# Kernel tuning notes

Measured on AMD Instinct MI355X. Metric: run time of the kernel, lower is better.

## Reference

```python
import jax, jax.numpy as jnp
import numpy as np

B, N, L = 64, 512, 768
M, K, H = 24, 30, 1024


def setup_inputs() -> dict:
    key = jax.random.key(0)
    ks = jax.random.split(key, 7)
    sent_embedding = jax.random.normal(ks[0], (B, N, L), dtype=jnp.float32)
    entity_embedding = jax.random.normal(ks[1], (B, M, K, H), dtype=jnp.float32)
    entity_embedding_mask = jax.random.bernoulli(ks[2], 0.1, (B, M, K))
    # -1 denotes a padded (absent) alias, as handled by select_alias_word_sent
    start_span_idx = jax.random.randint(ks[3], (B, M), -1, N, dtype=jnp.int32)
    end_span_idx = jax.random.randint(ks[4], (B, M), -1, N, dtype=jnp.int32)
    W_span = jax.random.normal(ks[5], (2 * L, H), dtype=jnp.float32) * (1.0 / np.sqrt(2 * L))
    b_span = jnp.zeros((H,), dtype=jnp.float32)
    return {
        "sent_embedding": sent_embedding,
        "entity_embedding": entity_embedding,
        "entity_embedding_mask": entity_embedding_mask,
        "start_span_idx": start_span_idx,
        "end_span_idx": end_span_idx,
        "W_span": W_span,
        "b_span": b_span,
    }


def _select_alias_word_sent(idx, sent):
    # idx: (B, M) positions into sentence; -1 means padded alias -> zero vector
    pad = idx == -1                                   # (B, M)
    safe = jnp.where(pad, 0, idx)                     # (B, M)
    g = jnp.take_along_axis(sent, safe[:, :, None], axis=1)  # (B, M, L)
    return jnp.where(pad[:, :, None], 0.0, g)


def reference(sent_embedding, entity_embedding, entity_embedding_mask,
              start_span_idx, end_span_idx, W_span, b_span):
    # gather start/end word vectors of each alias span
    start_w = _select_alias_word_sent(start_span_idx, sent_embedding)  # (B, M, L)
    end_w = _select_alias_word_sent(end_span_idx, sent_embedding)      # (B, M, L)
    pair = jnp.concatenate([start_w, end_w], axis=-1)                  # (B, M, 2L)
    # span_proj: single linear layer 2L -> H
    alias_emb = pair @ W_span + b_span                                 # (B, M, H)
    # zero out masked candidates
    ent = jnp.where(entity_embedding_mask[..., None], 0.0, entity_embedding)  # (B,M,K,H)
    # per-candidate dot product (the tiny bmm in the original)
    final_scores = jnp.einsum("bmh,bmkh->bmk", alias_emb, ent)         # (B, M, K)
    return final_scores, ent
```

## Files before the change

### kernel.cpp

```cpp
#include <hip/hip_runtime.h>
#include <stdint.h>

#define B_   64
#define N_   512
#define L_   768
#define M_   24
#define K_   30
#define H_   1024
#define L2_  1536
#define BM_  (B_ * M_)
#define BMK_ (B_ * M_ * K_)

typedef __attribute__((ext_vector_type(8))) short bf16x8;
typedef __attribute__((ext_vector_type(4))) float f32x4;

__device__ __forceinline__ ushort f2bf(float f) {
    union { float f; uint32_t u; } v; v.f = f;
    uint32_t u = v.u + 0x7FFFu + ((v.u >> 16) & 1u);
    return (ushort)(u >> 16);
}

__global__ void detect_mask_kernel(const uint32_t* __restrict__ mw,
                                   int* __restrict__ flag) {
    __shared__ int f;
    if (threadIdx.x == 0) f = 0;
    __syncthreads();
    int local = 0;
    const int nw = BMK_ / 4;
    for (int i = threadIdx.x; i < nw; i += blockDim.x) {
        uint32_t v = mw[i];
        if (v != 0u && v != 1u && v != 0x3F800000u) local = 1;
    }
    if (local) f = 1;
    __syncthreads();
    if (threadIdx.x == 0) *flag = f;
}

__global__ __launch_bounds__(192) void gather_pair_bf16(
    const float* __restrict__ sent,
    const int*   __restrict__ sidx,
    const int*   __restrict__ eidx,
    ushort*      __restrict__ pairB) {

    const int bm = blockIdx.x;
    const int t  = threadIdx.x;
    const int l  = t * 8;
    const int b  = bm / M_;

    int idx, ll;
    if (l < L_) { idx = sidx[bm]; ll = l; }
    else        { idx = eidx[bm]; ll = l - L_; }

    float4 v0 = make_float4(0.f, 0.f, 0.f, 0.f), v1 = v0;
    if (idx >= 0) {
        const float* src = sent + ((size_t)(b * N_ + idx)) * L_ + ll;
        v0 = *reinterpret_cast<const float4*>(src);
        v1 = *reinterpret_cast<const float4*>(src + 4);
    }
    ushort o[8] = { f2bf(v0.x), f2bf(v0.y), f2bf(v0.z), f2bf(v0.w),
                    f2bf(v1.x), f2bf(v1.y), f2bf(v1.z), f2bf(v1.w) };
    *reinterpret_cast<uint4*>(pairB + (size_t)bm * L2_ + l) =
        *reinterpret_cast<const uint4*>(o);
}

__global__ __launch_bounds__(256) void wt_bf16_kernel(
    const float* __restrict__ W, ushort* __restrict__ Wt) {

    __shared__ ushort tile[32][33];
    const int l0 = blockIdx.x * 32;
    const int h0 = blockIdx.y * 32;
    const int t  = threadIdx.x;

    {
        const int r  = t >> 3;
        const int c4 = (t & 7) * 4;
        const float4 v = *reinterpret_cast<const float4*>(
            W + (size_t)(l0 + r) * H_ + h0 + c4);
        tile[r][c4 + 0] = f2bf(v.x);
        tile[r][c4 + 1] = f2bf(v.y);
        tile[r][c4 + 2] = f2bf(v.z);
        tile[r][c4 + 3] = f2bf(v.w);
    }
    __syncthreads();
    {
        const int hr = t >> 3;
        const int l4 = (t & 7) * 4;
        ushort4 o;
        o.x = tile[l4 + 0][hr];
        o.y = tile[l4 + 1][hr];
        o.z = tile[l4 + 2][hr];
        o.w = tile[l4 + 3][hr];
        *reinterpret_cast<ushort4*>(Wt + (size_t)(h0 + hr) * L2_ + l0 + l4) = o;
    }
}

__global__ __launch_bounds__(64) void mfma_span_gemm(
    const ushort* __restrict__ pairB,
    const ushort* __restrict__ WtB,
    const float*  __restrict__ bias,
    float*        __restrict__ alias_out) {

    const int lane = threadIdx.x;
    const int lr = lane & 15;
    const int lg = lane >> 4;
    const int c0 = blockIdx.x * 32;
    const int r0 = blockIdx.y * 32;

    f32x4 acc00 = {}, acc01 = {}, acc10 = {}, acc11 = {};

    const ushort* a0 = pairB + (size_t)(r0 + lr) * L2_ + lg * 8;
    const ushort* a1 = a0 + 16 * L2_;
    const ushort* b0 = WtB   + (size_t)(c0 + lr) * L2_ + lg * 8;
    const ushort* b1 = b0 + 16 * L2_;

#pragma unroll 4
    for (int k0 = 0; k0 < L2_; k0 += 32) {
        const bf16x8 av0 = *reinterpret_cast<const bf16x8*>(a0 + k0);
        const bf16x8 av1 = *reinterpret_cast<const bf16x8*>(a1 + k0);
        const bf16x8 bv0 = *reinterpret_cast<const bf16x8*>(b0 + k0);
        const bf16x8 bv1 = *reinterpret_cast<const bf16x8*>(b1 + k0);
        acc00 = __builtin_amdgcn_mfma_f32_16x16x32_bf16(av0, bv0, acc00, 0, 0, 0);
        acc01 = __builtin_amdgcn_mfma_f32_16x16x32_bf16(av0, bv1, acc01, 0, 0, 0);
        acc10 = __builtin_amdgcn_mfma_f32_16x16x32_bf16(av1, bv0, acc10, 0, 0, 0);
        acc11 = __builtin_amdgcn_mfma_f32_16x16x32_bf16(av1, bv1, acc11, 0, 0, 0);
    }

    const float bj0 = bias[c0 + lr];
    const float bj1 = bias[c0 + 16 + lr];
#pragma unroll
    for (int q = 0; q < 4; ++q) {
        const size_t rA = (size_t)(r0 + lg * 4 + q) * H_;
        const size_t rB = (size_t)(r0 + 16 + lg * 4 + q) * H_;
        alias_out[rA + c0 + lr]      = acc00[q] + bj0;
        alias_out[rA + c0 + 16 + lr] = acc01[q] + bj1;
        alias_out[rB + c0 + lr]      = acc10[q] + bj0;
        alias_out[rB + c0 + 16 + lr] = acc11[q] + bj1;
    }
}

__global__ __launch_bounds__(256) void span_gemm_kernel(
    const float* __restrict__ sent,
    const int*   __restrict__ sidx,
    const int*   __restrict__ eidx,
    const float* __restrict__ W,
    const float* __restrict__ bias,
    float*       __restrict__ alias_out) {

    __shared__ float As[16][64];
    __shared__ float Bs[16][64];
    __shared__ int   offS[64];
    __shared__ int   offE[64];

    const int tid = threadIdx.x;
    const int bm0 = blockIdx.y * 64;
    const int h0  = blockIdx.x * 64;

    if (tid < 64) {
        const int bm = bm0 + tid;
        const int b  = bm / M_;
        const int si = sidx[bm];
        const int ei = eidx[bm];
        offS[tid] = (si < 0) ? -1 : (b * N_ + si) * L_;
        offE[tid] = (ei < 0) ? -1 : (b * N_ + ei) * L_;
    }
    __syncthreads();

    float acc[4][4] = {};
    const int ar  = tid >> 2;
    const int akq = (tid & 3) * 4;
    const int bkr = tid >> 4;
    const int bc  = (tid & 15) * 4;
    const int ty  = tid >> 4;
    const int tx  = tid & 15;

    for (int l0 = 0; l0 < L2_; l0 += 16) {
        {
            const int lb = l0 + akq;
            int off, ll;
            if (lb < L_) { off = offS[ar]; ll = lb; }
            else         { off = offE[ar]; ll = lb - L_; }
            float4 v;
            if (off < 0) v = make_float4(0.f, 0.f, 0.f, 0.f);
            else         v = *reinterpret_cast<const float4*>(sent + off + ll);
            As[akq + 0][ar] = v.x;  As[akq + 1][ar] = v.y;
            As[akq + 2][ar] = v.z;  As[akq + 3][ar] = v.w;
        }
        {
            const float4 v = *reinterpret_cast<const float4*>(
                W + (size_t)(l0 + bkr) * H_ + h0 + bc);
            *reinterpret_cast<float4*>(&Bs[bkr][bc]) = v;
        }
        __syncthreads();
#pragma unroll
        for (int k = 0; k < 16; ++k) {
            const float4 av = *reinterpret_cast<const float4*>(&As[k][ty * 4]);
            const float4 bv = *reinterpret_cast<const float4*>(&Bs[k][tx * 4]);
            acc[0][0] += av.x * bv.x; acc[0][1] += av.x * bv.y;
            acc[0][2] += av.x * bv.z; acc[0][3] += av.x * bv.w;
            acc[1][0] += av.y * bv.x; acc[1][1] += av.y * bv.y;
            acc[1][2] += av.y * bv.z; acc[1][3] += av.y * bv.w;
            acc[2][0] += av.z * bv.x; acc[2][1] += av.z * bv.y;
            acc[2][2] += av.z * bv.z; acc[2][3] += av.z * bv.w;
            acc[3][0] += av.w * bv.x; acc[3][1] += av.w * bv.y;
            acc[3][2] += av.w * bv.z; acc[3][3] += av.w * bv.w;
        }
        __syncthreads();
    }

    const float4 bb = *reinterpret_cast<const float4*>(bias + h0 + tx * 4);
#pragma unroll
    for (int i = 0; i < 4; ++i) {
        const int bm = bm0 + ty * 4 + i;
        const float4 o = make_float4(acc[i][0] + bb.x, acc[i][1] + bb.y,
                                     acc[i][2] + bb.z, acc[i][3] + bb.w);
        *reinterpret_cast<float4*>(alias_out + (size_t)bm * H_ + h0 + tx * 4) = o;
    }
}

__global__ __launch_bounds__(256) void ent_scores_kernel(
    const float* __restrict__ ent_in,
    const float* __restrict__ alias,
    const void*  __restrict__ mask,
    const int*   __restrict__ flag,
    float*       __restrict__ scores,
    float*       __restrict__ ent_out) {

    const int bmk = blockIdx.x;
    const int tid = threadIdx.x;

    const bool byte_packed = (*flag != 0);
    bool masked;
    if (byte_packed) masked = ((const uint8_t*)mask)[bmk] != 0;
    else             masked = ((const uint32_t*)mask)[bmk] != 0u;

    const size_t rowo = (size_t)bmk * H_;
    float p = 0.f;
    float4 e;
    if (masked) {
        e = make_float4(0.f, 0.f, 0.f, 0.f);
    } else {
        e = *reinterpret_cast<const float4*>(ent_in + rowo + tid * 4);
        const int bm = bmk / K_;
        const float4 a = *reinterpret_cast<const float4*>(
            alias + (size_t)bm * H_ + tid * 4);
        p = a.x * e.x + a.y * e.y + a.z * e.z + a.w * e.w;
    }
    *reinterpret_cast<float4*>(ent_out + rowo + tid * 4) = e;

#pragma unroll
    for (int off = 32; off > 0; off >>= 1) p += __shfl_down(p, off);
    __shared__ float red[4];
    if ((tid & 63) == 0) red[tid >> 6] = p;
    __syncthreads();
    if (tid == 0) scores[bmk] = red[0] + red[1] + red[2] + red[3];
}

extern "C" void kernel_launch(void* const* d_in, const int* in_sizes, int n_in,
                              void* d_out, int out_size, void* d_ws, size_t ws_size,
                              hipStream_t stream) {
    const float* sent = (const float*)d_in[0];
    const float* ent  = (const float*)d_in[1];
    const void*  mask = d_in[2];
    const int*   sidx = (const int*)d_in[3];
    const int*   eidx = (const int*)d_in[4];
    const float* W    = (const float*)d_in[5];
    const float* bias = (const float*)d_in[6];

    float* scores  = (float*)d_out;
    float* ent_out = (float*)d_out + (size_t)BMK_;

    const size_t ALIAS_B = (size_t)BM_ * H_ * 4;
    const size_t PAIR_B  = (size_t)BM_ * L2_ * 2;
    const size_t WT_B    = (size_t)H_ * L2_ * 2;

    int*    flag  = (int*)d_ws;
    float*  alias = (float*)((char*)d_ws + 256);
    ushort* pairB = (ushort*)((char*)d_ws + 256 + ALIAS_B);
    ushort* WtB   = (ushort*)((char*)d_ws + 256 + ALIAS_B + PAIR_B);

    detect_mask_kernel<<<1, 256, 0, stream>>>((const uint32_t*)mask, flag);

    if (ws_size >= 256 + ALIAS_B + PAIR_B + WT_B) {
        gather_pair_bf16<<<BM_, 192, 0, stream>>>(sent, sidx, eidx, pairB);
        wt_bf16_kernel<<<dim3(L2_ / 32, H_ / 32), 256, 0, stream>>>(W, WtB);
        mfma_span_gemm<<<dim3(H_ / 32, BM_ / 32), 64, 0, stream>>>(
            pairB, WtB, bias, alias);
    } else {
        span_gemm_kernel<<<dim3(H_ / 64, BM_ / 64), 256, 0, stream>>>(
            sent, sidx, eidx, W, bias, alias);
    }

    ent_scores_kernel<<<BMK_, 256, 0, stream>>>(
        ent, alias, mask, flag, scores, ent_out);
}
```

Baseline: 419.8 us.

## Merge prep kernels into one launch and use wave-per-row persistent entity scoring

Folds the mask-format detection, span gather/bf16 conversion and W transpose into a single prep kernel that picks its role from the block index, removing two launches. Replaces the one-block-per-row entity scoring kernel with a grid-stride kernel that assigns one wavefront per row, so no shared memory or block barrier is needed and masked rows skip the entity load. The single-block mask detection now runs alongside the other prep blocks rather than as its own serialized launch, though it can still be the slowest block and hold up the prep kernel.

After: 424.2 us. Within noise of the previous version (+1.0%).

```diff
diff --git a/kernel.cpp b/kernel.cpp
--- a/kernel.cpp
+++ b/kernel.cpp
@@ -36,61 +36,77 @@
     if (threadIdx.x == 0) *flag = f;
 }
 
-__global__ __launch_bounds__(192) void gather_pair_bf16(
+__global__ __launch_bounds__(256) void prep_kernel(
     const float* __restrict__ sent,
     const int*   __restrict__ sidx,
     const int*   __restrict__ eidx,
-    ushort*      __restrict__ pairB) {
-
-    const int bm = blockIdx.x;
-    const int t  = threadIdx.x;
-    const int l  = t * 8;
-    const int b  = bm / M_;
-
-    int idx, ll;
-    if (l < L_) { idx = sidx[bm]; ll = l; }
-    else        { idx = eidx[bm]; ll = l - L_; }
-
-    float4 v0 = make_float4(0.f, 0.f, 0.f, 0.f), v1 = v0;
-    if (idx >= 0) {
-        const float* src = sent + ((size_t)(b * N_ + idx)) * L_ + ll;
-        v0 = *reinterpret_cast<const float4*>(src);
-        v1 = *reinterpret_cast<const float4*>(src + 4);
-    }
-    ushort o[8] = { f2bf(v0.x), f2bf(v0.y), f2bf(v0.z), f2bf(v0.w),
-                    f2bf(v1.x), f2bf(v1.y), f2bf(v1.z), f2bf(v1.w) };
-    *reinterpret_cast<uint4*>(pairB + (size_t)bm * L2_ + l) =
-        *reinterpret_cast<const uint4*>(o);
-}
-
-__global__ __launch_bounds__(256) void wt_bf16_kernel(
-    const float* __restrict__ W, ushort* __restrict__ Wt) {
-
-    __shared__ ushort tile[32][33];
-    const int l0 = blockIdx.x * 32;
-    const int h0 = blockIdx.y * 32;
-    const int t  = threadIdx.x;
-
-    {
-        const int r  = t >> 3;
-        const int c4 = (t & 7) * 4;
-        const float4 v = *reinterpret_cast<const float4*>(
-            W + (size_t)(l0 + r) * H_ + h0 + c4);
-        tile[r][c4 + 0] = f2bf(v.x);
-        tile[r][c4 + 1] = f2bf(v.y);
-        tile[r][c4 + 2] = f2bf(v.z);
-        tile[r][c4 + 3] = f2bf(v.w);
-    }
-    __syncthreads();
-    {
-        const int hr = t >> 3;
-        const int l4 = (t & 7) * 4;
-        ushort4 o;
-        o.x = tile[l4 + 0][hr];
-        o.y = tile[l4 + 1][hr];
-        o.z = tile[l4 + 2][hr];
-        o.w = tile[l4 + 3][hr];
-        *reinterpret_cast<ushort4*>(Wt + (size_t)(h0 + hr) * L2_ + l0 + l4) = o;
+    const float* __restrict__ W,
+    const uint32_t* __restrict__ maskw,
+    ushort*      __restrict__ pairB,
+    ushort*      __restrict__ Wt,
+    int*         __restrict__ flag) {
+
+    const int blk = blockIdx.x;
+    const int t   = threadIdx.x;
+
+    if (blk < BM_) {
+        if (t < 192) {
+            const int bm = blk;
+            const int l  = t * 8;
+            const int b  = bm / M_;
+            int idx, ll;
+            if (l < L_) { idx = sidx[bm]; ll = l; }
+            else        { idx = eidx[bm]; ll = l - L_; }
+            float4 v0 = make_float4(0.f, 0.f, 0.f, 0.f), v1 = v0;
+            if (idx >= 0) {
+                const float* src = sent + ((size_t)(b * N_ + idx)) * L_ + ll;
+                v0 = *reinterpret_cast<const float4*>(src);
+                v1 = *reinterpret_cast<const float4*>(src + 4);
+            }
+            ushort o[8] = { f2bf(v0.x), f2bf(v0.y), f2bf(v0.z), f2bf(v0.w),
+                            f2bf(v1.x), f2bf(v1.y), f2bf(v1.z), f2bf(v1.w) };
+            *reinterpret_cast<uint4*>(pairB + (size_t)bm * L2_ + l) =
+                *reinterpret_cast<const uint4*>(o);
+        }
+    } else if (blk < BM_ + (L2_ / 32) * (H_ / 32)) {
+        __shared__ ushort tile[32][33];
+        const int idx = blk - BM_;
+        const int l0  = (idx % (L2_ / 32)) * 32;
+        const int h0  = (idx / (L2_ / 32)) * 32;
+        {
+            const int r  = t >> 3;
+            const int c4 = (t & 7) * 4;
+            const float4 v = *reinterpret_cast<const float4*>(
+                W + (size_t)(l0 + r) * H_ + h0 + c4);
+            tile[r][c4 + 0] = f2bf(v.x);
+            tile[r][c4 + 1] = f2bf(v.y);
+            tile[r][c4 + 2] = f2bf(v.z);
+            tile[r][c4 + 3] = f2bf(v.w);
+        }
+        __syncthreads();
+        {
+            const int hr = t >> 3;
+            const int l4 = (t & 7) * 4;
+            ushort4 o;
+            o.x = tile[l4 + 0][hr];
+            o.y = tile[l4 + 1][hr];
+            o.z = tile[l4 + 2][hr];
+            o.w = tile[l4 + 3][hr];
+            *reinterpret_cast<ushort4*>(Wt + (size_t)(h0 + hr) * L2_ + l0 + l4) = o;
+        }
+    } else {
+        __shared__ int f;
+        if (t == 0) f = 0;
+        __syncthreads();
+        int local = 0;
+        const int nw = BMK_ / 4;
+        for (int i = t; i < nw; i += blockDim.x) {
+            uint32_t v = maskw[i];
+            if (v != 0u && v != 1u && v != 0x3F800000u) local = 1;
+        }
+        if (local) f = 1;
+        __syncthreads();
+        if (t == 0) *flag = f;
     }
 }
 
@@ -135,6 +151,51 @@
         alias_out[rA + c0 + 16 + lr] = acc01[q] + bj1;
         alias_out[rB + c0 + lr]      = acc10[q] + bj0;
         alias_out[rB + c0 + 16 + lr] = acc11[q] + bj1;
+    }
+}
+
+#define ES_BLOCKS 1536
+__global__ __launch_bounds__(256) void ent_scores_v2(
+    const float* __restrict__ ent_in,
+    const float* __restrict__ alias,
+    const void*  __restrict__ mask,
+    const int*   __restrict__ flag,
+    float*       __restrict__ scores,
+    float*       __restrict__ ent_out) {
+
+    const int lane  = threadIdx.x & 63;
+    const int wid   = blockIdx.x * 4 + (threadIdx.x >> 6);
+    const int nwave = ES_BLOCKS * 4;
+
+    const bool byte_packed = (*flag != 0);
+    const uint8_t*  mb = (const uint8_t*)mask;
+    const uint32_t* mw = (const uint32_t*)mask;
+
+    for (int row = wid; row < BMK_; row += nwave) {
+        const bool masked = byte_packed ? (mb[row] != 0) : (mw[row] != 0u);
+        const size_t rowo = (size_t)row * H_;
+        const int bm = row / K_;
+
+        float p = 0.f;
+        if (masked) {
+            const float4 z = make_float4(0.f, 0.f, 0.f, 0.f);
+#pragma unroll
+            for (int c = 0; c < 4; ++c)
+                *reinterpret_cast<float4*>(ent_out + rowo + c * 256 + lane * 4) = z;
+        } else {
+#pragma unroll
+            for (int c = 0; c < 4; ++c) {
+                const int off = c * 256 + lane * 4;
+                const float4 e = *reinterpret_cast<const float4*>(ent_in + rowo + off);
+                const float4 a = *reinterpret_cast<const float4*>(
+                    alias + (size_t)bm * H_ + off);
+                p += a.x * e.x + a.y * e.y + a.z * e.z + a.w * e.w;
+                *reinterpret_cast<float4*>(ent_out + rowo + off) = e;
+            }
+        }
+#pragma unroll
+        for (int off = 32; off > 0; off >>= 1) p += __shfl_down(p, off);
+        if (lane == 0) scores[row] = p;
     }
 }
 
@@ -217,44 +278,6 @@
     }
 }
 
-__global__ __launch_bounds__(256) void ent_scores_kernel(
-    const float* __restrict__ ent_in,
-    const float* __restrict__ alias,
-    const void*  __restrict__ mask,
-    const int*   __restrict__ flag,
-    float*       __restrict__ scores,
-    float*       __restrict__ ent_out) {
-
-    const int bmk = blockIdx.x;
-    const int tid = threadIdx.x;
-
-    const bool byte_packed = (*flag != 0);
-    bool masked;
-    if (byte_packed) masked = ((const uint8_t*)mask)[bmk] != 0;
-    else             masked = ((const uint32_t*)mask)[bmk] != 0u;
-
-    const size_t rowo = (size_t)bmk * H_;
-    float p = 0.f;
-    float4 e;
-    if (masked) {
-        e = make_float4(0.f, 0.f, 0.f, 0.f);
-    } else {
-        e = *reinterpret_cast<const float4*>(ent_in + rowo + tid * 4);
-        const int bm = bmk / K_;
-        const float4 a = *reinterpret_cast<const float4*>(
-            alias + (size_t)bm * H_ + tid * 4);
-        p = a.x * e.x + a.y * e.y + a.z * e.z + a.w * e.w;
-    }
-    *reinterpret_cast<float4*>(ent_out + rowo + tid * 4) = e;
-
-#pragma unroll
-    for (int off = 32; off > 0; off >>= 1) p += __shfl_down(p, off);
-    __shared__ float red[4];
-    if ((tid & 63) == 0) red[tid >> 6] = p;
-    __syncthreads();
-    if (tid == 0) scores[bmk] = red[0] + red[1] + red[2] + red[3];
-}
-
 extern "C" void kernel_launch(void* const* d_in, const int* in_sizes, int n_in,
                               void* d_out, int out_size, void* d_ws, size_t ws_size,
                               hipStream_t stream) {
@@ -278,18 +301,18 @@
     ushort* pairB = (ushort*)((char*)d_ws + 256 + ALIAS_B);
     ushort* WtB   = (ushort*)((char*)d_ws + 256 + ALIAS_B + PAIR_B);
 
-    detect_mask_kernel<<<1, 256, 0, stream>>>((const uint32_t*)mask, flag);
-
     if (ws_size >= 256 + ALIAS_B + PAIR_B + WT_B) {
-        gather_pair_bf16<<<BM_, 192, 0, stream>>>(sent, sidx, eidx, pairB);
-        wt_bf16_kernel<<<dim3(L2_ / 32, H_ / 32), 256, 0, stream>>>(W, WtB);
+        const int nprep = BM_ + (L2_ / 32) * (H_ / 32) + 1;
+        prep_kernel<<<nprep, 256, 0, stream>>>(
+            sent, sidx, eidx, W, (const uint32_t*)mask, pairB, WtB, flag);
         mfma_span_gemm<<<dim3(H_ / 32, BM_ / 32), 64, 0, stream>>>(
             pairB, WtB, bias, alias);
     } else {
+        detect_mask_kernel<<<1, 256, 0, stream>>>((const uint32_t*)mask, flag);
         span_gemm_kernel<<<dim3(H_ / 64, BM_ / 64), 256, 0, stream>>>(
             sent, sidx, eidx, W, bias, alias);
     }
 
-    ent_scores_kernel<<<BMK_, 256, 0, stream>>>(
+    ent_scores_v2<<<ES_BLOCKS, 256, 0, stream>>>(
         ent, alias, mask, flag, scores, ent_out);
 }
```
